# Performance work log

Measured on AMD Instinct MI355X. Metric: run time of the kernel, lower is better.

## Reference

```python
import jax, jax.numpy as jnp
import numpy as np

BIG = 10000.0

def setup_inputs() -> dict:
    key = jax.random.key(0)
    k1, k2, k3 = jax.random.split(key, 3)
    B, S, D = 32, 4096, 512
    x = jax.random.normal(k1, (B, S, D), dtype=jnp.float32)
    mask = jax.random.randint(k2, (B, S), 0, 2).astype(bool)
    w_attn = jax.random.normal(k3, (D, 1), dtype=jnp.float32)
    return {"x": x, "mask": mask, "w_attn": w_attn}

def reference(x, mask, w_attn):
    # x: [B, S, D], mask: [B, S] bool, w_attn: [D, 1]
    mask_f = mask.astype(jnp.float32)[:, :, None]          # [B, S, 1]
    masked_x = x * mask_f
    seq_len = jnp.sum(mask_f, axis=1) + 1e-6               # [B, 1]
    mean_pool = jnp.sum(masked_x, axis=1) / seq_len        # [B, D]

    m3 = mask[:, :, None]
    max_pool = jnp.max(jnp.where(m3, x, -BIG), axis=1)     # [B, D]
    min_pool = jnp.min(jnp.where(m3, x, BIG), axis=1)      # [B, D]

    attn_scores = jnp.einsum('bsd,do->bso', x, w_attn)     # [B, S, 1]
    attn_scores = jnp.where(m3, attn_scores, -BIG)
    attn_w = jax.nn.softmax(attn_scores, axis=1)           # [B, S, 1]
    attn_pool = jnp.sum(x * attn_w, axis=1)                # [B, D]

    return jnp.concatenate([mean_pool, max_pool, min_pool, attn_pool], axis=-1)
```

## Files before the change

### kernel.cpp

```cpp
#include <hip/hip_runtime.h>
#include <math.h>

#define BIGV 10000.0f

constexpr int B = 32, S = 4096, D = 512;
constexpr int C   = 32;
constexpr int L   = S / C;
constexpr int WPB = 4;
constexpr int RW  = L / WPB;
constexpr int NREC = B * C * WPB;
constexpr int RPB  = C * WPB;

__global__ __launch_bounds__(256, 4)
void pool_stream(const float* __restrict__ x, const int* __restrict__ mask,
                 const float* __restrict__ wvec, float* __restrict__ ws) {
  const int tid = threadIdx.x, lane = tid & 63, w = tid >> 6;
  const int blk = blockIdx.x, b = blk / C, c = blk % C;
  const int s0 = c * L + w * RW;

  const float4* xrow4 = (const float4*)(x + ((size_t)b * S + s0) * D);
  const int*    mr    = mask + (size_t)b * S + s0;

  const float4* wv4 = (const float4*)wvec;
  const float4  w0 = wv4[lane * 2], w1 = wv4[lane * 2 + 1];

  float m = -INFINITY, l = 0.f, cnt = 0.f;
  float o[8], sm[8], mx[8], mn[8];
  #pragma unroll
  for (int j = 0; j < 8; ++j) { o[j] = 0.f; sm[j] = 0.f; mx[j] = -BIGV; mn[j] = BIGV; }

  float4 a0 = xrow4[lane * 2];
  float4 a1 = xrow4[lane * 2 + 1];
  int    mb = mr[0];

  for (int r = 0; r < RW; ++r) {
    const float4 c0 = a0, c1 = a1; const int cm = mb;
    if (r + 1 < RW) {
      a0 = xrow4[(size_t)(r + 1) * (D / 4) + lane * 2];
      a1 = xrow4[(size_t)(r + 1) * (D / 4) + lane * 2 + 1];
      mb = mr[r + 1];
    }
    float d = 0.f;
    d = fmaf(c0.x, w0.x, d); d = fmaf(c0.y, w0.y, d);
    d = fmaf(c0.z, w0.z, d); d = fmaf(c0.w, w0.w, d);
    d = fmaf(c1.x, w1.x, d); d = fmaf(c1.y, w1.y, d);
    d = fmaf(c1.z, w1.z, d); d = fmaf(c1.w, w1.w, d);
    #pragma unroll
    for (int off = 32; off; off >>= 1) d += __shfl_xor(d, off, 64);

    const float s = cm ? d : -BIGV;
    const float m_new = fmaxf(m, s);
    if (m_new > m) {
      const float alpha = __expf(m - m_new);
      l *= alpha;
      #pragma unroll
      for (int j = 0; j < 8; ++j) o[j] *= alpha;
      m = m_new;
    }
    const float p = __expf(s - m);
    l += p;
    const float mskf = cm ? 1.f : 0.f;
    cnt += mskf;

    const float xa[8] = {c0.x, c0.y, c0.z, c0.w, c1.x, c1.y, c1.z, c1.w};
    #pragma unroll
    for (int j = 0; j < 8; ++j) {
      o[j]  = fmaf(p, xa[j], o[j]);
      sm[j] = fmaf(mskf, xa[j], sm[j]);
      mx[j] = fmaxf(mx[j], cm ? xa[j] : -BIGV);
      mn[j] = fminf(mn[j], cm ? xa[j] :  BIGV);
    }
  }

  const size_t rec = (size_t)blk * WPB + w;
  float4* po = (float4*)(ws + rec * D);
  float4* ps = (float4*)(ws + (size_t)NREC * D + rec * D);
  float4* px = (float4*)(ws + 2 * (size_t)NREC * D + rec * D);
  float4* pn = (float4*)(ws + 3 * (size_t)NREC * D + rec * D);
  po[lane * 2]     = make_float4(o[0], o[1], o[2], o[3]);
  po[lane * 2 + 1] = make_float4(o[4], o[5], o[6], o[7]);
  ps[lane * 2]     = make_float4(sm[0], sm[1], sm[2], sm[3]);
  ps[lane * 2 + 1] = make_float4(sm[4], sm[5], sm[6], sm[7]);
  px[lane * 2]     = make_float4(mx[0], mx[1], mx[2], mx[3]);
  px[lane * 2 + 1] = make_float4(mx[4], mx[5], mx[6], mx[7]);
  pn[lane * 2]     = make_float4(mn[0], mn[1], mn[2], mn[3]);
  pn[lane * 2 + 1] = make_float4(mn[4], mn[5], mn[6], mn[7]);
  if (lane == 0) {
    float* scal = ws + 4 * (size_t)NREC * D;
    scal[rec]            = m;
    scal[NREC + rec]     = l;
    scal[2 * NREC + rec] = cnt;
  }
}

__global__ __launch_bounds__(512)
void pool_merge(const float* __restrict__ ws, float* __restrict__ out) {
  const int b = blockIdx.x, tid = threadIdx.x;
  const float* scal = ws + 4 * (size_t)NREC * D;
  const int r0 = b * RPB;

  float m_f = -INFINITY;
  #pragma unroll 4
  for (int i = 0; i < RPB; ++i) m_f = fmaxf(m_f, scal[r0 + i]);

  float Lsum = 0.f, CNT = 0.f;
  float o = 0.f, sm = 0.f, mx = -BIGV, mn = BIGV;
  #pragma unroll 4
  for (int i = 0; i < RPB; ++i) {
    const size_t rec = (size_t)(r0 + i);
    const float a = __expf(scal[rec] - m_f);
    Lsum += scal[NREC + rec] * a;
    CNT  += scal[2 * NREC + rec];
    o  = fmaf(ws[rec * D + tid], a, o);
    sm += ws[(size_t)NREC * D + rec * D + tid];
    mx  = fmaxf(mx, ws[2 * (size_t)NREC * D + rec * D + tid]);
    mn  = fminf(mn, ws[3 * (size_t)NREC * D + rec * D + tid]);
  }
  float* ob = out + (size_t)b * 4 * D;
  ob[tid]         = sm / (CNT + 1e-6f);
  ob[D + tid]     = mx;
  ob[2 * D + tid] = mn;
  ob[3 * D + tid] = o / Lsum;
}

extern "C" void kernel_launch(void* const* d_in, const int* in_sizes, int n_in,
                              void* d_out, int out_size, void* d_ws, size_t ws_size,
                              hipStream_t stream) {
  const float* x    = (const float*)d_in[0];
  const int*   mask = (const int*)d_in[1];
  const float* w    = (const float*)d_in[2];
  float* out = (float*)d_out;
  float* ws  = (float*)d_ws;

  pool_stream<<<dim3(B * C), dim3(256), 0, stream>>>(x, mask, w, ws);
  pool_merge<<<dim3(B), dim3(512), 0, stream>>>(ws, out);
}
```

Baseline: 389.4 us.

## Merge warp partials in shared memory and widen merge kernel grid

```diff
diff --git a/kernel.cpp b/kernel.cpp
--- a/kernel.cpp
+++ b/kernel.cpp
@@ -4,42 +4,49 @@
 #define BIGV 10000.0f
 
 constexpr int B = 32, S = 4096, D = 512;
-constexpr int C   = 32;
-constexpr int L   = S / C;
-constexpr int WPB = 4;
-constexpr int RW  = L / WPB;
-constexpr int NREC = B * C * WPB;
-constexpr int RPB  = C * WPB;
+constexpr int C    = 32;
+constexpr int L    = S / C;
+constexpr int WPB  = 4;
+constexpr int RW   = L / WPB;
+constexpr int NREC = B * C;
+constexpr int RPB  = C;
 
 __global__ __launch_bounds__(256, 4)
 void pool_stream(const float* __restrict__ x, const int* __restrict__ mask,
                  const float* __restrict__ wvec, float* __restrict__ ws) {
+  __shared__ float ls_o[WPB][D];
+  __shared__ float ls_sm[WPB][D];
+  __shared__ float ls_mx[WPB][D];
+  __shared__ float ls_mn[WPB][D];
+  __shared__ float ls_m[WPB], ls_l[WPB], ls_c[WPB];
+
   const int tid = threadIdx.x, lane = tid & 63, w = tid >> 6;
   const int blk = blockIdx.x, b = blk / C, c = blk % C;
   const int s0 = c * L + w * RW;
 
-  const float4* xrow4 = (const float4*)(x + ((size_t)b * S + s0) * D);
-  const int*    mr    = mask + (size_t)b * S + s0;
+  const float4* row4 = (const float4*)(x + ((size_t)b * S + s0) * D);
+  const int*    mr   = mask + (size_t)b * S + s0;
 
   const float4* wv4 = (const float4*)wvec;
-  const float4  w0 = wv4[lane * 2], w1 = wv4[lane * 2 + 1];
+  const float4  w0 = wv4[lane], w1 = wv4[64 + lane];
 
   float m = -INFINITY, l = 0.f, cnt = 0.f;
   float o[8], sm[8], mx[8], mn[8];
   #pragma unroll
   for (int j = 0; j < 8; ++j) { o[j] = 0.f; sm[j] = 0.f; mx[j] = -BIGV; mn[j] = BIGV; }
 
-  float4 a0 = xrow4[lane * 2];
-  float4 a1 = xrow4[lane * 2 + 1];
-  int    mb = mr[0];
+  float4 cur0 = row4[lane],       cur1 = row4[64 + lane];        int curm = mr[0];
+  float4 nx0  = row4[128 + lane], nx1  = row4[192 + lane];       int nxm  = mr[1];
 
   for (int r = 0; r < RW; ++r) {
-    const float4 c0 = a0, c1 = a1; const int cm = mb;
-    if (r + 1 < RW) {
-      a0 = xrow4[(size_t)(r + 1) * (D / 4) + lane * 2];
-      a1 = xrow4[(size_t)(r + 1) * (D / 4) + lane * 2 + 1];
-      mb = mr[r + 1];
+    const float4 c0 = cur0, c1 = cur1; const int cm = curm;
+    cur0 = nx0; cur1 = nx1; curm = nxm;
+    if (r + 2 < RW) {
+      nx0 = row4[(size_t)(r + 2) * (D / 4) + lane];
+      nx1 = row4[(size_t)(r + 2) * (D / 4) + 64 + lane];
+      nxm = mr[r + 2];
     }
+
     float d = 0.f;
     d = fmaf(c0.x, w0.x, d); d = fmaf(c0.y, w0.y, d);
     d = fmaf(c0.z, w0.z, d); d = fmaf(c0.w, w0.w, d);
@@ -72,35 +79,60 @@
     }
   }
 
-  const size_t rec = (size_t)blk * WPB + w;
-  float4* po = (float4*)(ws + rec * D);
-  float4* ps = (float4*)(ws + (size_t)NREC * D + rec * D);
-  float4* px = (float4*)(ws + 2 * (size_t)NREC * D + rec * D);
-  float4* pn = (float4*)(ws + 3 * (size_t)NREC * D + rec * D);
-  po[lane * 2]     = make_float4(o[0], o[1], o[2], o[3]);
-  po[lane * 2 + 1] = make_float4(o[4], o[5], o[6], o[7]);
-  ps[lane * 2]     = make_float4(sm[0], sm[1], sm[2], sm[3]);
-  ps[lane * 2 + 1] = make_float4(sm[4], sm[5], sm[6], sm[7]);
-  px[lane * 2]     = make_float4(mx[0], mx[1], mx[2], mx[3]);
-  px[lane * 2 + 1] = make_float4(mx[4], mx[5], mx[6], mx[7]);
-  pn[lane * 2]     = make_float4(mn[0], mn[1], mn[2], mn[3]);
-  pn[lane * 2 + 1] = make_float4(mn[4], mn[5], mn[6], mn[7]);
-  if (lane == 0) {
+  ((float4*)ls_o[w])[lane]       = make_float4(o[0], o[1], o[2], o[3]);
+  ((float4*)ls_o[w])[64 + lane]  = make_float4(o[4], o[5], o[6], o[7]);
+  ((float4*)ls_sm[w])[lane]      = make_float4(sm[0], sm[1], sm[2], sm[3]);
+  ((float4*)ls_sm[w])[64 + lane] = make_float4(sm[4], sm[5], sm[6], sm[7]);
+  ((float4*)ls_mx[w])[lane]      = make_float4(mx[0], mx[1], mx[2], mx[3]);
+  ((float4*)ls_mx[w])[64 + lane] = make_float4(mx[4], mx[5], mx[6], mx[7]);
+  ((float4*)ls_mn[w])[lane]      = make_float4(mn[0], mn[1], mn[2], mn[3]);
+  ((float4*)ls_mn[w])[64 + lane] = make_float4(mn[4], mn[5], mn[6], mn[7]);
+  if (lane == 0) { ls_m[w] = m; ls_l[w] = l; ls_c[w] = cnt; }
+  __syncthreads();
+
+  float m_blk = fmaxf(fmaxf(ls_m[0], ls_m[1]), fmaxf(ls_m[2], ls_m[3]));
+  float al[WPB];
+  float l_f = 0.f, c_f = 0.f;
+  #pragma unroll
+  for (int k = 0; k < WPB; ++k) {
+    al[k] = __expf(ls_m[k] - m_blk);
+    l_f += ls_l[k] * al[k];
+    c_f += ls_c[k];
+  }
+  #pragma unroll
+  for (int h = 0; h < 2; ++h) {
+    const int col = h * 256 + tid;
+    float of = 0.f, sf = 0.f, xf = -BIGV, nf = BIGV;
+    #pragma unroll
+    for (int k = 0; k < WPB; ++k) {
+      of = fmaf(ls_o[k][col], al[k], of);
+      sf += ls_sm[k][col];
+      xf  = fmaxf(xf, ls_mx[k][col]);
+      nf  = fminf(nf, ls_mn[k][col]);
+    }
+    const size_t rec = (size_t)blk;
+    ws[rec * D + col]                      = of;
+    ws[(size_t)NREC * D + rec * D + col]   = sf;
+    ws[2 * (size_t)NREC * D + rec * D + col] = xf;
+    ws[3 * (size_t)NREC * D + rec * D + col] = nf;
+  }
+  if (tid == 0) {
     float* scal = ws + 4 * (size_t)NREC * D;
-    scal[rec]            = m;
-    scal[NREC + rec]     = l;
-    scal[2 * NREC + rec] = cnt;
+    scal[blk]            = m_blk;
+    scal[NREC + blk]     = l_f;
+    scal[2 * NREC + blk] = c_f;
   }
 }
 
-__global__ __launch_bounds__(512)
+__global__ __launch_bounds__(128)
 void pool_merge(const float* __restrict__ ws, float* __restrict__ out) {
-  const int b = blockIdx.x, tid = threadIdx.x;
+  const int b = blockIdx.x, q = blockIdx.y, tid = threadIdx.x;
+  const int col = q * 128 + tid;
   const float* scal = ws + 4 * (size_t)NREC * D;
   const int r0 = b * RPB;
 
   float m_f = -INFINITY;
-  #pragma unroll 4
+  #pragma unroll 8
   for (int i = 0; i < RPB; ++i) m_f = fmaxf(m_f, scal[r0 + i]);
 
   float Lsum = 0.f, CNT = 0.f;
@@ -111,16 +143,16 @@
     const float a = __expf(scal[rec] - m_f);
     Lsum += scal[NREC + rec] * a;
     CNT  += scal[2 * NREC + rec];
-    o  = fmaf(ws[rec * D + tid], a, o);
-    sm += ws[(size_t)NREC * D + rec * D + tid];
-    mx  = fmaxf(mx, ws[2 * (size_t)NREC * D + rec * D + tid]);
-    mn  = fminf(mn, ws[3 * (size_t)NREC * D + rec * D + tid]);
+    o  = fmaf(ws[rec * D + col], a, o);
+    sm += ws[(size_t)NREC * D + rec * D + col];
+    mx  = fmaxf(mx, ws[2 * (size_t)NREC * D + rec * D + col]);
+    mn  = fminf(mn, ws[3 * (size_t)NREC * D + rec * D + col]);
   }
   float* ob = out + (size_t)b * 4 * D;
-  ob[tid]         = sm / (CNT + 1e-6f);
-  ob[D + tid]     = mx;
-  ob[2 * D + tid] = mn;
-  ob[3 * D + tid] = o / Lsum;
+  ob[col]         = sm / (CNT + 1e-6f);
+  ob[D + col]     = mx;
+  ob[2 * D + col] = mn;
+  ob[3 * D + col] = o / Lsum;
 }
 
 extern "C" void kernel_launch(void* const* d_in, const int* in_sizes, int n_in,
@@ -133,5 +165,5 @@
   float* ws  = (float*)d_ws;
 
   pool_stream<<<dim3(B * C), dim3(256), 0, stream>>>(x, mask, w, ws);
-  pool_merge<<<dim3(B), dim3(512), 0, stream>>>(ws, out);
+  pool_merge<<<dim3(B, 4), dim3(128), 0, stream>>>(ws, out);
 }
```

New measurement: 365.3 us. 1.07x faster.
